# Kernel optimization log

Measured on AMD Instinct MI355X. Metric: run time of the kernel, lower is better.

The kernel has to match this reference:

```python
import jax, jax.numpy as jnp
import numpy as np

N_HEAD = 16
D_MODEL = 1024
HEAD_SIZE = D_MODEL // N_HEAD
BATCH, SEQ = 2, 2048


def setup_inputs() -> dict:
    key = jax.random.key(0)
    ks = jax.random.split(key, 11)
    s = 1.0 / np.sqrt(D_MODEL)
    inp = {
        "query": jax.random.normal(ks[0], (BATCH, SEQ, D_MODEL), jnp.float32),
        "key_in": jax.random.normal(ks[1], (BATCH, SEQ, D_MODEL), jnp.float32),
        "value": jax.random.normal(ks[2], (BATCH, SEQ, D_MODEL), jnp.float32),
        # per-head Q/K/V projections stacked: [n_head, d_model, head_size]
        "Wq": jax.random.uniform(ks[3], (N_HEAD, D_MODEL, HEAD_SIZE), jnp.float32, -s, s),
        "Wk": jax.random.uniform(ks[4], (N_HEAD, D_MODEL, HEAD_SIZE), jnp.float32, -s, s),
        "Wv": jax.random.uniform(ks[5], (N_HEAD, D_MODEL, HEAD_SIZE), jnp.float32, -s, s),
        "bq": jax.random.uniform(ks[6], (N_HEAD, HEAD_SIZE), jnp.float32, -s, s),
        "bk": jax.random.uniform(ks[7], (N_HEAD, HEAD_SIZE), jnp.float32, -s, s),
        "bv": jax.random.uniform(ks[8], (N_HEAD, HEAD_SIZE), jnp.float32, -s, s),
        "Wo": jax.random.uniform(ks[9], (D_MODEL, D_MODEL), jnp.float32, -s, s),
        "bo": jax.random.uniform(ks[10], (D_MODEL,), jnp.float32, -s, s),
    }
    return inp


def reference(query, key_in, value, Wq, Wk, Wv, bq, bk, bv, Wo, bo):
    # Per-head projections fused into one einsum each: [b, h, s, k]
    Q = jnp.einsum("bsd,hdk->bhsk", query, Wq) + bq[:, None, :]
    K = jnp.einsum("bsd,hdk->bhsk", key_in, Wk) + bk[:, None, :]
    V = jnp.einsum("bsd,hdk->bhsk", value, Wv) + bv[:, None, :]
    scale = 1.0 / np.sqrt(HEAD_SIZE)
    wei = jnp.einsum("bhqk,bhsk->bhqs", Q, K) * scale  # [b, h, s, s]
    wei = jax.nn.softmax(wei, axis=-1)
    out = jnp.einsum("bhqs,bhsk->bhqk", wei, V)  # [b, h, s, k]
    b, h, s, k = out.shape
    out = out.transpose(0, 2, 1, 3).reshape(b, s, h * k)
    return out @ Wo.T + bo
```

## Files before the change

kernel.cpp:

```cpp
#include <hip/hip_runtime.h>
#include <hip/hip_bf16.h>

typedef __attribute__((ext_vector_type(8))) short short8;
typedef __attribute__((ext_vector_type(4))) short bf16x4;
typedef __attribute__((ext_vector_type(4))) float f32x4;

#define DM 1024
#define NH 16
#define HS 64
#define SEQL 2048

__device__ __forceinline__ float bf2f(short s) {
  unsigned u = ((unsigned)(unsigned short)s) << 16;
  float f;
  __builtin_memcpy(&f, &u, 4);
  return f;
}
__device__ __forceinline__ short f2bf(float f) {
  unsigned u;
  __builtin_memcpy(&u, &f, 4);
  u = u + 0x7FFFu + ((u >> 16) & 1u);
  return (short)(u >> 16);
}

__device__ __forceinline__ void gl2lds16(const void* g, void* l) {
  __builtin_amdgcn_global_load_lds(
      (const __attribute__((address_space(1))) void*)g,
      (__attribute__((address_space(3))) void*)l, 16, 0, 0);
}

__device__ __forceinline__ short8 cvt_pk8(f32x4 lo, f32x4 hi) {
  union { short8 s8; unsigned u[4]; } r;
  asm("v_cvt_pk_bf16_f32 %0, %1, %2" : "=v"(r.u[0]) : "v"(lo[0]), "v"(lo[1]));
  asm("v_cvt_pk_bf16_f32 %0, %1, %2" : "=v"(r.u[1]) : "v"(lo[2]), "v"(lo[3]));
  asm("v_cvt_pk_bf16_f32 %0, %1, %2" : "=v"(r.u[2]) : "v"(hi[0]), "v"(hi[1]));
  asm("v_cvt_pk_bf16_f32 %0, %1, %2" : "=v"(r.u[3]) : "v"(hi[2]), "v"(hi[3]));
  return r.s8;
}

__global__ __launch_bounds__(256) void pack_w_kernel(
    const float* __restrict__ Wq, const float* __restrict__ Wk, const float* __restrict__ Wv,
    short* __restrict__ WtQ, short* __restrict__ WtK, short* __restrict__ WtV) {
  const float* W = (blockIdx.z == 0) ? Wq : (blockIdx.z == 1) ? Wk : Wv;
  short* Wt      = (blockIdx.z == 0) ? WtQ : (blockIdx.z == 1) ? WtK : WtV;
  __shared__ short Ts[64][73];
  const int h = blockIdx.y, dm0 = blockIdx.x * 64;
  const int tid = threadIdx.x;
#pragma unroll
  for (int p = 0; p < 4; ++p) {
    int idx = p * 256 + tid;
    int i = idx >> 4, hsq = (idx & 15) * 4;
    f32x4 v = *(const f32x4*)&W[((h << 10) + dm0 + i) * 64 + hsq];
#pragma unroll
    for (int j = 0; j < 4; ++j) Ts[i][hsq + j] = f2bf(v[j]);
  }
  __syncthreads();
  {
    int hs = tid >> 2, dmq = (tid & 3) * 16;
    short8 o0, o1;
#pragma unroll
    for (int j = 0; j < 8; ++j) { o0[j] = Ts[dmq + j][hs]; o1[j] = Ts[dmq + 8 + j][hs]; }
    short* dst = &Wt[((h * 64 + hs) << 10) + dm0 + dmq];
    *(short8*)dst = o0;
    *(short8*)(dst + 8) = o1;
  }
}

__global__ __launch_bounds__(256) void cvt_bf16_kernel(const float* __restrict__ in,
                                                       short* __restrict__ out) {
  int i = blockIdx.x * 256 + threadIdx.x;
  const f32x4* p = (const f32x4*)(in + (size_t)i * 8);
  f32x4 a = p[0], b = p[1];
  short8 o;
#pragma unroll
  for (int j = 0; j < 4; ++j) { o[j] = f2bf(a[j]); o[4 + j] = f2bf(b[j]); }
  *(short8*)(out + (size_t)i * 8) = o;
}

struct GemmArgs {
  const void* A;
  const void* Bt;
  const float* bias;
  short* out;
  float* outf;
  int mode;
};

template <bool AF32, int NB>
__global__ __launch_bounds__(256) void gemm_bt_kernel(GemmArgs g0, GemmArgs g1, GemmArgs g2) {
  GemmArgs g = (blockIdx.z == 0) ? g0 : (blockIdx.z == 1) ? g1 : g2;
  const int K = 1024;
  const int TN = NB * 32;
  const int m0 = blockIdx.x * 128;
  const int n0 = blockIdx.y * TN;
  const int tid = threadIdx.x;
  const int w = tid >> 6, l = tid & 63, lr = l & 15, lk = l >> 4;
  const int wr = w >> 1, wc = w & 1;

  __shared__ __align__(16) char AsRaw[128 * 32 * (AF32 ? 4 : 2)];
  __shared__ __align__(16) short Bs[TN * 32];
  float* Asf = (float*)AsRaw;
  short* As  = (short*)AsRaw;

  const int swz3 = lr & 7;
  const int swz2 = (lr & 3) ^ ((lr >> 2) & 3);

  f32x4 acc[4][NB];
#pragma unroll
  for (int i = 0; i < 4; ++i)
#pragma unroll
    for (int j = 0; j < NB; ++j) acc[i][j] = (f32x4){0.f, 0.f, 0.f, 0.f};

  for (int k0 = 0; k0 < K; k0 += 32) {
    __syncthreads();
    if constexpr (AF32) {
      const float* Af = (const float*)g.A;
#pragma unroll
      for (int i = 0; i < 4; ++i) {
        int c = i * 256 + tid;
        int row = c >> 3, s = c & 7;
        int gc = (s ^ (row & 7)) * 4;
        gl2lds16(&Af[(size_t)(m0 + row) * K + k0 + gc], &Asf[c * 4]);
      }
    } else {
      const short* Ah = (const short*)g.A;
#pragma unroll
      for (int i = 0; i < 2; ++i) {
        int c = i * 256 + tid;
        int row = c >> 2, s = c & 3;
        int gc = (s ^ ((row & 3) ^ ((row >> 2) & 3))) * 8;
        gl2lds16(&Ah[(size_t)(m0 + row) * K + k0 + gc], &As[c * 8]);
      }
    }
    {
      const short* Bh = (const short*)g.Bt;
#pragma unroll
      for (int i = 0; i < TN / 64; ++i) {
        int c = i * 256 + tid;
        int row = c >> 2, s = c & 3;
        int gc = (s ^ ((row & 3) ^ ((row >> 2) & 3))) * 8;
        gl2lds16(&Bh[(size_t)(n0 + row) * K + k0 + gc], &Bs[c * 8]);
      }
    }
    __syncthreads();

    short8 af[4], bfr[NB];
#pragma unroll
    for (int t = 0; t < 4; ++t) {
      int row = wr * 64 + t * 16 + lr;
      if constexpr (AF32) {
        int base = row * 32;
        f32x4 lo = *(const f32x4*)&Asf[base + (((lk << 1)    ) ^ swz3) * 4];
        f32x4 hi = *(const f32x4*)&Asf[base + (((lk << 1) | 1) ^ swz3) * 4];
        af[t] = cvt_pk8(lo, hi);
      } else {
        af[t] = *(const short8*)&As[row * 32 + (lk ^ swz2) * 8];
      }
    }
#pragma unroll
    for (int t = 0; t < NB; ++t) {
      int row = wc * (NB * 16) + t * 16 + lr;
      bfr[t] = *(const short8*)&Bs[row * 32 + (lk ^ swz2) * 8];
    }
#pragma unroll
    for (int ti = 0; ti < 4; ++ti)
#pragma unroll
      for (int tj = 0; tj < NB; ++tj)
        acc[ti][tj] = __builtin_amdgcn_mfma_f32_16x16x32_bf16(af[ti], bfr[tj], acc[ti][tj], 0, 0, 0);
  }

#pragma unroll
  for (int ti = 0; ti < 4; ++ti)
#pragma unroll
    for (int tj = 0; tj < NB; ++tj) {
      int n = n0 + wc * (NB * 16) + tj * 16 + lr;
      float bia = g.bias[n];
      int mb = m0 + wr * 64 + ti * 16 + lk * 4;
      if (g.mode == 2) {
        bf16x4 o;
#pragma unroll
        for (int r = 0; r < 4; ++r) o[r] = f2bf(acc[ti][tj][r] + bia);
        *(bf16x4*)&g.out[((mb >> 11) * 16 + (n >> 6)) * (SEQL * HS) + (n & 63) * SEQL + (mb & 2047)] = o;
      } else {
#pragma unroll
        for (int r = 0; r < 4; ++r) {
          int m = mb + r;
          float v = acc[ti][tj][r] + bia;
          if (g.mode == 0) {
            g.out[((m >> 11) * 16 + (n >> 6)) * (SEQL * HS) + (m & 2047) * HS + (n & 63)] = f2bf(v);
          } else {
            g.outf[(size_t)m * DM + n] = v;
          }
        }
      }
    }
}

__global__ __launch_bounds__(256, 4) void attn_kernel(const short* __restrict__ Qg, const short* __restrict__ Kg,
                                                      const short* __restrict__ Vtg, short* __restrict__ Og) {
  const int qt = blockIdx.x;
  const int bh = blockIdx.y;
  const short* Qp = Qg + bh * SEQL * HS;
  const short* Kp = Kg + bh * SEQL * HS;
  const short* Vp = Vtg + bh * HS * SEQL;
  const int tid = threadIdx.x, w = tid >> 6, l = tid & 63, lr = l & 15, lk = l >> 4;
  const int qw = qt * 64 + w * 16;

  __shared__ __align__(16) short Ks[128][72];
  __shared__ __align__(16) short Vt[64][136];

  short8 qf[2];
#pragma unroll
  for (int kk = 0; kk < 2; ++kk) {
    short8 qr = *(const short8*)&Qp[(qw + lr) * HS + kk * 32 + lk * 8];
#pragma unroll
    for (int j = 0; j < 8; ++j) qf[kk][j] = f2bf(bf2f(qr[j]) * 0.125f);
  }

  float mrow = -1e30f, lrow = 0.f;
  f32x4 accO[4];
#pragma unroll
  for (int t = 0; t < 4; ++t) accO[t] = (f32x4){0.f, 0.f, 0.f, 0.f};

  for (int kv = 0; kv < 16; ++kv) {
    __syncthreads();
#pragma unroll
    for (int i = 0; i < 4; ++i) {
      int q = tid + i * 256;
      int row = q >> 3, col = (q & 7) * 8;
      *(short8*)&Ks[row][col] = *(const short8*)&Kp[(kv * 128 + row) * HS + col];
    }
#pragma unroll
    for (int i = 0; i < 4; ++i) {
      int q = tid + i * 256;
      int d = q >> 4, sc = (q & 15) * 8;
      *(short8*)&Vt[d][sc] = *(const short8*)&Vp[d * SEQL + kv * 128 + sc];
    }
    __syncthreads();

    f32x4 accS[8];
#pragma unroll
    for (int tj = 0; tj < 8; ++tj) {
      short8 a0 = *(const short8*)&Ks[tj * 16 + lr][lk * 8];
      short8 a1 = *(const short8*)&Ks[tj * 16 + lr][32 + lk * 8];
      f32x4 z = (f32x4){0.f, 0.f, 0.f, 0.f};
      z = __builtin_amdgcn_mfma_f32_16x16x32_bf16(a0, qf[0], z, 0, 0, 0);
      accS[tj] = __builtin_amdgcn_mfma_f32_16x16x32_bf16(a1, qf[1], z, 0, 0, 0);
    }

    float mx = accS[0][0];
#pragma unroll
    for (int tj = 0; tj < 8; ++tj)
#pragma unroll
      for (int r = 0; r < 4; ++r) mx = fmaxf(mx, accS[tj][r]);
    mx = fmaxf(mx, __shfl_xor(mx, 16));
    mx = fmaxf(mx, __shfl_xor(mx, 32));
    float mn = fmaxf(mrow, mx);
    float alpha = __expf(mrow - mn);
    float ps = 0.f;
#pragma unroll
    for (int tj = 0; tj < 8; ++tj)
#pragma unroll
      for (int r = 0; r < 4; ++r) {
        float p = __expf(accS[tj][r] - mn);
        accS[tj][r] = p;
        ps += p;
      }
    ps += __shfl_xor(ps, 16);
    ps += __shfl_xor(ps, 32);
    lrow = lrow * alpha + ps;
    mrow = mn;
#pragma unroll
    for (int t = 0; t < 4; ++t) accO[t] *= alpha;

#pragma unroll
    for (int st = 0; st < 8; ++st) {
      bf16x4 bfrag;
#pragma unroll
      for (int r = 0; r < 4; ++r) bfrag[r] = f2bf(accS[st][r]);
#pragma unroll
      for (int tjd = 0; tjd < 4; ++tjd) {
        bf16x4 afrag = *(const bf16x4*)&Vt[tjd * 16 + lr][st * 16 + lk * 4];
        accO[tjd] = __builtin_amdgcn_mfma_f32_16x16x16bf16_1k(afrag, bfrag, accO[tjd], 0, 0, 0);
      }
    }
  }

  const int b = bh >> 4, h = bh & 15;
  float inv = 1.f / lrow;
  size_t rowbase = (size_t)(b * SEQL + qw + lr) * DM + h * HS;
#pragma unroll
  for (int tjd = 0; tjd < 4; ++tjd) {
    bf16x4 o;
#pragma unroll
    for (int r = 0; r < 4; ++r) o[r] = f2bf(accO[tjd][r] * inv);
    *(bf16x4*)&Og[rowbase + tjd * 16 + lk * 4] = o;
  }
}

extern "C" void kernel_launch(void* const* d_in, const int* in_sizes, int n_in,
                              void* d_out, int out_size, void* d_ws, size_t ws_size,
                              hipStream_t stream) {
  const float* query  = (const float*)d_in[0];
  const float* key_in = (const float*)d_in[1];
  const float* value  = (const float*)d_in[2];
  const float* Wq = (const float*)d_in[3];
  const float* Wk = (const float*)d_in[4];
  const float* Wv = (const float*)d_in[5];
  const float* bq = (const float*)d_in[6];
  const float* bk = (const float*)d_in[7];
  const float* bv = (const float*)d_in[8];
  const float* Wo = (const float*)d_in[9];
  const float* bo = (const float*)d_in[10];
  float* out = (float*)d_out;

  short* ws  = (short*)d_ws;
  short* Qb  = ws;
  short* Kb  = Qb + (4 << 20);
  short* Vbt = Kb + (4 << 20);
  short* X   = Vbt + (4 << 20);
  short* WtQ = X;
  short* WtK = WtQ + (1 << 20);
  short* WtV = WtK + (1 << 20);
  short* At  = X;
  short* Wob = Qb;

  pack_w_kernel<<<dim3(16, 16, 3), 256, 0, stream>>>(Wq, Wk, Wv, WtQ, WtK, WtV);

  GemmArgs gq{query, WtQ, bq, Qb, nullptr, 0}, gk{key_in, WtK, bk, Kb, nullptr, 0},
           gv{value, WtV, bv, Vbt, nullptr, 2};
  gemm_bt_kernel<true, 4><<<dim3(32, 8, 3), 256, 0, stream>>>(gq, gk, gv);

  attn_kernel<<<dim3(32, 32), 256, 0, stream>>>(Qb, Kb, Vbt, At);

  cvt_bf16_kernel<<<dim3(512), 256, 0, stream>>>(Wo, Wob);

  GemmArgs go{At, Wob, bo, nullptr, out, 1};
  gemm_bt_kernel<false, 2><<<dim3(32, 16, 1), 256, 0, stream>>>(go, go, go);
}
```

Baseline: 289.9 us.

## Double-buffer GEMM LDS tiles and register-prefetch K/V tiles in attention

The projection GEMM now uses two LDS buffers, so the next K-slice's global-to-LDS copy is issued before computing on the current slice, with one barrier per iteration instead of two. The attention kernel prefetches the next K/V tile into registers while computing on the current tile, then writes it to LDS at the top of the next iteration. This hides global load latency behind MFMA work. In exchange it doubles GEMM shared memory and raises register pressure in attention, whose occupancy hint drops from 4 to 3 blocks per CU.

```diff
diff --git a/kernel.cpp b/kernel.cpp
--- a/kernel.cpp
+++ b/kernel.cpp
@@ -97,10 +97,8 @@
   const int w = tid >> 6, l = tid & 63, lr = l & 15, lk = l >> 4;
   const int wr = w >> 1, wc = w & 1;
 
-  __shared__ __align__(16) char AsRaw[128 * 32 * (AF32 ? 4 : 2)];
-  __shared__ __align__(16) short Bs[TN * 32];
-  float* Asf = (float*)AsRaw;
-  short* As  = (short*)AsRaw;
+  __shared__ __align__(16) char AsRaw[2][128 * 32 * (AF32 ? 4 : 2)];
+  __shared__ __align__(16) short Bs[2][TN * 32];
 
   const int swz3 = lr & 7;
   const int swz2 = (lr & 3) ^ ((lr >> 2) & 3);
@@ -111,10 +109,10 @@
 #pragma unroll
     for (int j = 0; j < NB; ++j) acc[i][j] = (f32x4){0.f, 0.f, 0.f, 0.f};
 
-  for (int k0 = 0; k0 < K; k0 += 32) {
-    __syncthreads();
+  auto STAGE = [&](int buf, int k0) {
     if constexpr (AF32) {
       const float* Af = (const float*)g.A;
+      float* Asf = (float*)AsRaw[buf];
 #pragma unroll
       for (int i = 0; i < 4; ++i) {
         int c = i * 256 + tid;
@@ -124,6 +122,7 @@
       }
     } else {
       const short* Ah = (const short*)g.A;
+      short* As = (short*)AsRaw[buf];
 #pragma unroll
       for (int i = 0; i < 2; ++i) {
         int c = i * 256 + tid;
@@ -132,18 +131,19 @@
         gl2lds16(&Ah[(size_t)(m0 + row) * K + k0 + gc], &As[c * 8]);
       }
     }
-    {
-      const short* Bh = (const short*)g.Bt;
-#pragma unroll
-      for (int i = 0; i < TN / 64; ++i) {
-        int c = i * 256 + tid;
-        int row = c >> 2, s = c & 3;
-        int gc = (s ^ ((row & 3) ^ ((row >> 2) & 3))) * 8;
-        gl2lds16(&Bh[(size_t)(n0 + row) * K + k0 + gc], &Bs[c * 8]);
-      }
-    }
-    __syncthreads();
-
+    const short* Bh = (const short*)g.Bt;
+#pragma unroll
+    for (int i = 0; i < TN / 64; ++i) {
+      int c = i * 256 + tid;
+      int row = c >> 2, s = c & 3;
+      int gc = (s ^ ((row & 3) ^ ((row >> 2) & 3))) * 8;
+      gl2lds16(&Bh[(size_t)(n0 + row) * K + k0 + gc], &Bs[buf][c * 8]);
+    }
+  };
+
+  auto COMPUTE = [&](int buf) {
+    const float* Asf = (const float*)AsRaw[buf];
+    const short* As  = (const short*)AsRaw[buf];
     short8 af[4], bfr[NB];
 #pragma unroll
     for (int t = 0; t < 4; ++t) {
@@ -160,14 +160,25 @@
 #pragma unroll
     for (int t = 0; t < NB; ++t) {
       int row = wc * (NB * 16) + t * 16 + lr;
-      bfr[t] = *(const short8*)&Bs[row * 32 + (lk ^ swz2) * 8];
+      bfr[t] = *(const short8*)&Bs[buf][row * 32 + (lk ^ swz2) * 8];
     }
 #pragma unroll
     for (int ti = 0; ti < 4; ++ti)
 #pragma unroll
       for (int tj = 0; tj < NB; ++tj)
         acc[ti][tj] = __builtin_amdgcn_mfma_f32_16x16x32_bf16(af[ti], bfr[tj], acc[ti][tj], 0, 0, 0);
-  }
+  };
+
+  STAGE(0, 0);
+  __syncthreads();
+  int cur = 0;
+  for (int t = 0; t < 31; ++t) {
+    STAGE(cur ^ 1, (t + 1) * 32);
+    COMPUTE(cur);
+    __syncthreads();
+    cur ^= 1;
+  }
+  COMPUTE(cur);
 
 #pragma unroll
   for (int ti = 0; ti < 4; ++ti)
@@ -196,7 +207,7 @@
     }
 }
 
-__global__ __launch_bounds__(256, 4) void attn_kernel(const short* __restrict__ Qg, const short* __restrict__ Kg,
+__global__ __launch_bounds__(256, 3) void attn_kernel(const short* __restrict__ Qg, const short* __restrict__ Kg,
                                                       const short* __restrict__ Vtg, short* __restrict__ Og) {
   const int qt = blockIdx.x;
   const int bh = blockIdx.y;
@@ -222,21 +233,27 @@
 #pragma unroll
   for (int t = 0; t < 4; ++t) accO[t] = (f32x4){0.f, 0.f, 0.f, 0.f};
 
+  short8 kreg[4], vreg[4];
+  auto loadKV = [&](int kv) {
+#pragma unroll
+    for (int i = 0; i < 4; ++i) {
+      int q = tid + i * 256;
+      kreg[i] = *(const short8*)&Kp[(kv * 128 + (q >> 3)) * HS + (q & 7) * 8];
+      vreg[i] = *(const short8*)&Vp[(q >> 4) * SEQL + kv * 128 + (q & 15) * 8];
+    }
+  };
+  loadKV(0);
+
   for (int kv = 0; kv < 16; ++kv) {
     __syncthreads();
 #pragma unroll
     for (int i = 0; i < 4; ++i) {
       int q = tid + i * 256;
-      int row = q >> 3, col = (q & 7) * 8;
-      *(short8*)&Ks[row][col] = *(const short8*)&Kp[(kv * 128 + row) * HS + col];
-    }
-#pragma unroll
-    for (int i = 0; i < 4; ++i) {
-      int q = tid + i * 256;
-      int d = q >> 4, sc = (q & 15) * 8;
-      *(short8*)&Vt[d][sc] = *(const short8*)&Vp[d * SEQL + kv * 128 + sc];
+      *(short8*)&Ks[q >> 3][(q & 7) * 8] = kreg[i];
+      *(short8*)&Vt[q >> 4][(q & 15) * 8] = vreg[i];
     }
     __syncthreads();
+    if (kv < 15) loadKV(kv + 1);
 
     f32x4 accS[8];
 #pragma unroll
```

Result: faster. 259.7 us (-10.4%).
